# Optimization experiments

Hardware: AMD Instinct MI355X
Metric: run time of the kernel (lower is better)

## Reference

```python
import jax, jax.numpy as jnp
import numpy as np

VOCAB = 4194304
EMBED = 128
BATCH = 16384
NUM_DENSE = 13
NUM_CAT = 26
BOT_DIMS = (512, 256, 128)
TOP_DIMS = (1024, 1024, 512, 256, 1)


def _dense_params(key, fan_in, fan_out):
    kw, kb = jax.random.split(key)
    w = jax.random.normal(kw, (fan_in, fan_out), jnp.float32) * np.sqrt(2.0 / (fan_in + fan_out))
    b = jax.random.normal(kb, (fan_out,), jnp.float32) * np.sqrt(1.0 / fan_out)
    return w, b


def setup_inputs() -> dict:
    key = jax.random.key(0)
    ks = jax.random.split(key, 16)
    inp = {}
    inp['x_dense'] = jax.random.normal(ks[0], (BATCH, NUM_DENSE), jnp.float32)
    inp['x_cat'] = jax.random.randint(ks[1], (BATCH, NUM_CAT), 0, VOCAB, dtype=jnp.int32)
    # embedding table: uniform(0,1) * 1/sqrt(vocab)
    inp['embedding_table'] = jax.random.uniform(ks[2], (VOCAB, EMBED), jnp.float32) * np.float32(1.0 / np.sqrt(VOCAB))
    # bottom MLP params
    fan_in = NUM_DENSE
    for i, d in enumerate(BOT_DIMS):
        w, b = _dense_params(ks[3 + i], fan_in, d)
        inp[f'w_bot{i}'], inp[f'b_bot{i}'] = w, b
        fan_in = d
    # top MLP params; input dim = embed_dim + n_triu(27) = 128 + 378 = 506
    n_feat = 1 + NUM_CAT  # 27
    fan_in = EMBED + n_feat * (n_feat + 1) // 2
    for i, d in enumerate(TOP_DIMS):
        w, b = _dense_params(ks[8 + i], fan_in, d)
        inp[f'w_top{i}'], inp[f'b_top{i}'] = w, b
        fan_in = d
    return inp


def _forward(x_dense, x_cat, embedding_table,
             w_bot0, b_bot0, w_bot1, b_bot1, w_bot2, b_bot2,
             w_top0, b_top0, w_top1, b_top1, w_top2, b_top2,
             w_top3, b_top3, w_top4, b_top4):
    B = x_dense.shape[0]
    # bottom MLP
    h = x_dense
    for w, b in ((w_bot0, b_bot0), (w_bot1, b_bot1), (w_bot2, b_bot2)):
        h = jax.nn.relu(h @ w + b)
    bot_out = h  # [B, 128]
    feat = bot_out.reshape(B, -1, EMBED)  # [B, 1, 128]
    # embedding gather (irregular access)
    idx = (x_cat.reshape(-1) % VOCAB)
    emb = embedding_table[idx].reshape(B, NUM_CAT, EMBED)  # [B, 26, 128]
    stack = jnp.concatenate([feat, emb], axis=1)  # [B, 27, 128]
    # self interaction + upper-triangular (incl. diagonal) extraction
    xact = jnp.einsum('bnd,bmd->bnm', stack, stack)  # [B, 27, 27]
    i, j = jnp.triu_indices(stack.shape[1])
    inter = xact[:, i, j]  # [B, 378]
    top = jnp.concatenate([bot_out, inter], axis=-1)  # [B, 506]
    tops = ((w_top0, b_top0), (w_top1, b_top1), (w_top2, b_top2), (w_top3, b_top3), (w_top4, b_top4))
    for li, (w, b) in enumerate(tops):
        top = top @ w + b
        if li < len(tops) - 1:
            top = jax.nn.relu(top)
    return top  # [B, 1] logits


def reference(x_dense, x_cat, embedding_table,
              w_bot0, b_bot0, w_bot1, b_bot1, w_bot2, b_bot2,
              w_top0, b_top0, w_top1, b_top1, w_top2, b_top2,
              w_top3, b_top3, w_top4, b_top4):
    return _forward(x_dense, x_cat, embedding_table,
                    w_bot0, b_bot0, w_bot1, b_bot1, w_bot2, b_bot2,
                    w_top0, b_top0, w_top1, b_top1, w_top2, b_top2,
                    w_top3, b_top3, w_top4, b_top4)
```

## Files before the change

### kernel.cpp

```cpp
#include <hip/hip_runtime.h>
#include <cstdint>
#include <cstddef>

#define BATCH 16384
#define VOCAB_MASK (4194304 - 1)

typedef __attribute__((ext_vector_type(4))) float f32x4;
typedef __attribute__((ext_vector_type(8))) __bf16 bf16x8;
typedef __attribute__((ext_vector_type(4))) __bf16 bf16x4;

static_assert(sizeof(bf16x8) == 16, "bf16x8 must be 16 bytes");

static __device__ __forceinline__ __bf16 f2bf(float f) {
  union { float f; unsigned u; } in; in.f = f;
  unsigned r = in.u + 0x7FFF + ((in.u >> 16) & 1);
  union { unsigned short s; __bf16 b; } out; out.s = (unsigned short)(r >> 16);
  return out.b;
}
static __device__ __forceinline__ float bf2f(__bf16 b) {
  union { __bf16 b; unsigned short s; } in; in.b = b;
  union { unsigned u; float f; } out; out.u = ((unsigned)in.s) << 16;
  return out.f;
}

#define GLDS16(g, l) __builtin_amdgcn_global_load_lds( \
    (const __attribute__((address_space(1))) unsigned int*)(g), \
    (__attribute__((address_space(3))) unsigned int*)(l), 16, 0, 0)

static __device__ __forceinline__ unsigned swz16(unsigned b) {
  return b ^ ((((b >> 6) & 3u) ^ ((b >> 8) & 3u)) << 4);
}
static __device__ __forceinline__ bf16x8 lds_frag(const char* smem, unsigned base,
                                                  unsigned r, unsigned cg) {
  unsigned b = r * 64u + cg;
  return *(const bf16x8*)(smem + base + swz16(b));
}

struct TJob { const float* W; __bf16* WT; int K, N, Kp, tx, off; };
struct TJobs { TJob j[7]; };

__global__ __launch_bounds__(256) void transpose_all(TJobs js, int njobs)
{
  __shared__ float tile[64][65];
  int b = blockIdx.x;
  int ji = 0;
  #pragma unroll
  for (int i = 1; i < 7; ++i) if (i < njobs && b >= js.j[i].off) ji = i;
  const TJob jb = js.j[ji];
  int lb = b - jb.off;
  int bx = lb % jb.tx, by = lb / jb.tx;
  const int kb = bx * 64, nb = by * 64;
  const int tx = threadIdx.x & 63, ty = threadIdx.x >> 6;
  #pragma unroll
  for (int i = 0; i < 64; i += 4) {
    int k = kb + ty + i, n = nb + tx;
    tile[ty + i][tx] = (k < jb.K && n < jb.N) ? jb.W[(size_t)k * jb.N + n] : 0.f;
  }
  __syncthreads();
  #pragma unroll
  for (int i = 0; i < 64; i += 4) {
    int n = nb + ty + i, k = kb + tx;
    if (n < jb.N && k < jb.Kp) jb.WT[(size_t)n * jb.Kp + k] = f2bf(tile[tx][ty + i]);
  }
}

__global__ __launch_bounds__(256) void bottom_interact(
    const float* __restrict__ x, const int* __restrict__ xcat,
    const float* __restrict__ emb,
    const __bf16* __restrict__ w0t, const float* __restrict__ b0,
    const __bf16* __restrict__ w1t, const float* __restrict__ b1,
    const __bf16* __restrict__ w2t, const float* __restrict__ b2,
    __bf16* __restrict__ top_in)
{
  __shared__ __align__(16) char smem[77824];
  const int tid = threadIdx.x, lane = tid & 63, w = tid >> 6;
  const int r0 = blockIdx.x * 32;
  const int srow_b = lane >> 2;
  const int scol_b = (lane & 3) * 8;
  const unsigned rA = lane & 15, cgw = (lane >> 4) * 8;

  #define AS_B(r,c) (smem + 8704  + (r)*80   + (c)*2)
  #define BS_B(r,c) (smem + 11264 + (r)*64   + (c)*2)
  #define H1_B(r,c) (smem + 27648 + (r)*528  + (c)*2)
  #define H0_B(r,c) (smem + 44544 + (r)*1040 + (c)*2)
  #define H2_B(r,c) (smem +         (r)*272  + (c)*2)

  auto ld_gather = [&](float4 (&buf)[13], int s) {
    const int* xs = xcat + (size_t)(r0 + w * 8 + s) * 26;
    #pragma unroll
    for (int i = 0; i < 13; ++i) {
      int fi = 2 * i + (lane >> 5);
      int ridx = xs[fi] & VOCAB_MASK;
      buf[i] = *(const float4*)(emb + (size_t)ridx * 128 + (lane & 31) * 4);
    }
  };
  float4 bufA[13], bufB[13];
  ld_gather(bufA, 0);

  for (int idx = tid; idx < 32 * 40; idx += 256) {
    int row = idx / 40, k = idx - row * 40;
    float v = (k < 13) ? x[(size_t)(r0 + row) * 13 + k] : 0.f;
    *(__bf16*)AS_B(row, k) = f2bf(v);
  }

  #pragma unroll
  for (int p = 0; p < 2; ++p) {
    __syncthreads();
    #pragma unroll
    for (int c = 0; c < 4; ++c) {
      int row = w * 64 + c * 16 + srow_b;
      GLDS16(w0t + (size_t)(p * 256 + row) * 32 + scol_b, BS_B(row, scol_b));
    }
    __syncthreads();
    bf16x8 a[2], bv[4];
    #pragma unroll
    for (int m = 0; m < 2; ++m) a[m] = *(const bf16x8*)AS_B(rA + m * 16, cgw);
    #pragma unroll
    for (int n = 0; n < 4; ++n) bv[n] = *(const bf16x8*)BS_B(w * 64 + n * 16 + rA, cgw);
    f32x4 acc[2][4] = {};
    #pragma unroll
    for (int m = 0; m < 2; ++m)
      #pragma unroll
      for (int n = 0; n < 4; ++n)
        acc[m][n] = __builtin_amdgcn_mfma_f32_16x16x32_bf16(a[m], bv[n], acc[m][n], 0, 0, 0);
    #pragma unroll
    for (int m = 0; m < 2; ++m)
      #pragma unroll
      for (int n = 0; n < 4; ++n) {
        int col = p * 256 + w * 64 + n * 16 + (int)rA;
        float bb = b0[col];
        #pragma unroll
        for (int r = 0; r < 4; ++r) {
          int row = m * 16 + (lane >> 4) * 4 + r;
          *(__bf16*)H0_B(row, col) = f2bf(fmaxf(acc[m][n][r] + bb, 0.f));
        }
      }
  }

  f32x4 acc1[2][4] = {};
  for (int k0 = 0; k0 < 512; k0 += 32) {
    __syncthreads();
    #pragma unroll
    for (int c = 0; c < 4; ++c) {
      int row = w * 64 + c * 16 + srow_b;
      GLDS16(w1t + (size_t)row * 512 + k0 + scol_b, BS_B(row, scol_b));
    }
    __syncthreads();
    bf16x8 a[2], bv[4];
    #pragma unroll
    for (int m = 0; m < 2; ++m) a[m] = *(const bf16x8*)H0_B(rA + m * 16, k0 + cgw);
    #pragma unroll
    for (int n = 0; n < 4; ++n) bv[n] = *(const bf16x8*)BS_B(w * 64 + n * 16 + rA, cgw);
    #pragma unroll
    for (int m = 0; m < 2; ++m)
      #pragma unroll
      for (int n = 0; n < 4; ++n)
        acc1[m][n] = __builtin_amdgcn_mfma_f32_16x16x32_bf16(a[m], bv[n], acc1[m][n], 0, 0, 0);
  }
  #pragma unroll
  for (int m = 0; m < 2; ++m)
    #pragma unroll
    for (int n = 0; n < 4; ++n) {
      int col = w * 64 + n * 16 + (int)rA;
      float bb = b1[col];
      #pragma unroll
      for (int r = 0; r < 4; ++r) {
        int row = m * 16 + (lane >> 4) * 4 + r;
        *(__bf16*)H1_B(row, col) = f2bf(fmaxf(acc1[m][n][r] + bb, 0.f));
      }
    }

  f32x4 acc2[2][2] = {};
  for (int k0 = 0; k0 < 256; k0 += 32) {
    __syncthreads();
    #pragma unroll
    for (int c = 0; c < 2; ++c) {
      int row = w * 32 + c * 16 + srow_b;
      GLDS16(w2t + (size_t)row * 256 + k0 + scol_b, BS_B(row, scol_b));
    }
    __syncthreads();
    bf16x8 a[2], bv[2];
    #pragma unroll
    for (int m = 0; m < 2; ++m) a[m] = *(const bf16x8*)H1_B(rA + m * 16, k0 + cgw);
    #pragma unroll
    for (int n = 0; n < 2; ++n) bv[n] = *(const bf16x8*)BS_B(w * 32 + n * 16 + rA, cgw);
    #pragma unroll
    for (int m = 0; m < 2; ++m)
      #pragma unroll
      for (int n = 0; n < 2; ++n)
        acc2[m][n] = __builtin_amdgcn_mfma_f32_16x16x32_bf16(a[m], bv[n], acc2[m][n], 0, 0, 0);
  }
  #pragma unroll
  for (int m = 0; m < 2; ++m)
    #pragma unroll
    for (int n = 0; n < 2; ++n) {
      int col = w * 32 + n * 16 + (int)rA;
      float bb = b2[col];
      #pragma unroll
      for (int r = 0; r < 4; ++r) {
        int row = m * 16 + (lane >> 4) * 4 + r;
        *(__bf16*)H2_B(row, col) = f2bf(fmaxf(acc2[m][n][r] + bb, 0.f));
      }
    }

  __syncthreads();

  char* st_w = smem + 8704 + (unsigned)w * 8704u;
  #pragma unroll
  for (int r = 27; r < 32; ++r) *(unsigned*)(st_w + r * 272 + lane * 4) = 0;

  #pragma unroll
  for (int s = 0; s < 8; ++s) {
    float4 (&cur)[13] = (s & 1) ? bufB : bufA;
    float4 (&nxt)[13] = (s & 1) ? bufA : bufB;
    const int sg = r0 + w * 8 + s;
    __bf16* op = top_in + (size_t)sg * 512;

    unsigned hv = *(const unsigned*)(smem + (unsigned)(w * 8 + s) * 272u + lane * 4);
    *(unsigned*)(st_w + lane * 4) = hv;
    ((unsigned*)op)[lane] = hv;
    if (lane < 3) ((unsigned*)op)[253 + lane] = 0;

    #pragma unroll
    for (int i = 0; i < 13; ++i) {
      int row = 1 + 2 * i + (lane >> 5);
      float4 v = cur[i];
      bf16x4 bv;
      bv[0] = f2bf(v.x); bv[1] = f2bf(v.y); bv[2] = f2bf(v.z); bv[3] = f2bf(v.w);
      *(bf16x4*)(st_w + row * 272 + (lane & 31) * 8) = bv;
    }
    if (s < 7) ld_gather(nxt, s + 1);

    asm volatile("s_waitcnt lgkmcnt(0)" ::: "memory");
    __builtin_amdgcn_sched_barrier(0);

    f32x4 a00 = {}, a01 = {}, a11 = {};
    #pragma unroll
    for (int k0 = 0; k0 < 4; ++k0) {
      bf16x8 fr0 = *(const bf16x8*)(st_w + (lane & 15) * 272 + k0 * 64 + (lane >> 4) * 16);
      bf16x8 fr1 = *(const bf16x8*)(st_w + (16 + (lane & 15)) * 272 + k0 * 64 + (lane >> 4) * 16);
      a00 = __builtin_amdgcn_mfma_f32_16x16x32_bf16(fr0, fr0, a00, 0, 0, 0);
      a01 = __builtin_amdgcn_mfma_f32_16x16x32_bf16(fr0, fr1, a01, 0, 0, 0);
      a11 = __builtin_amdgcn_mfma_f32_16x16x32_bf16(fr1, fr1, a11, 0, 0, 0);
    }

    const int jc = lane & 15, rb = (lane >> 4) * 4;
    #pragma unroll
    for (int r = 0; r < 4; ++r) {
      {
        int i = rb + r, j = jc;
        if (i <= j) op[128 + i * 27 - i * (i - 1) / 2 + (j - i)] = f2bf(a00[r]);
      }
      {
        int i = rb + r, j = 16 + jc;
        if (j <= 26) op[128 + i * 27 - i * (i - 1) / 2 + (j - i)] = f2bf(a01[r]);
      }
      {
        int i = 16 + rb + r, j = 16 + jc;
        if (i <= j && j <= 26) op[128 + i * 27 - i * (i - 1) / 2 + (j - i)] = f2bf(a11[r]);
      }
    }
  }
  #undef AS_B
  #undef BS_B
  #undef H1_B
  #undef H0_B
  #undef H2_B
}

__global__ __launch_bounds__(512, 2) void gemm_8ph(
    const __bf16* __restrict__ A, const __bf16* __restrict__ WT,
    const float* __restrict__ bias, __bf16* __restrict__ C,
    int N, int sA, int K, int gm)
{
  __shared__ __align__(16) char smem[65536];
  const int tid = threadIdx.x, lane = tid & 63, w = tid >> 6;
  const int wm = w >> 2, wn = w & 3;

  int nb = gridDim.x;
  int id = blockIdx.x;
  int swz = ((nb & 7) == 0) ? ((id & 7) * (nb >> 3) + (id >> 3)) : id;
  const int m0 = (swz % gm) * 256, n0 = (swz / gm) * 256;

  unsigned Ld[2]; const __bf16* sAp[2]; const __bf16* sBp[2];
  #pragma unroll
  for (int h = 0; h < 2; ++h) {
    unsigned L = h * 8192u + (unsigned)w * 1024u + (unsigned)lane * 16u;
    unsigned Ls = swz16(L);
    Ld[h] = L;
    int srow = Ls >> 6, scb = Ls & 63;
    sAp[h] = A  + (size_t)(m0 + srow) * sA + (scb >> 1);
    sBp[h] = WT + (size_t)(n0 + srow) * K  + (scb >> 1);
  }

  #define STAGE_A(kt, p) { GLDS16(sAp[0] + (kt)*32, smem + (p)*32768 + Ld[0]); \
                           GLDS16(sAp[1] + (kt)*32, smem + (p)*32768 + Ld[1]); }
  #define STAGE_B(kt, p) { GLDS16(sBp[0] + (kt)*32, smem + (p)*32768 + 16384 + Ld[0]); \
                           GLDS16(sBp[1] + (kt)*32, smem + (p)*32768 + 16384 + Ld[1]); }

  const unsigned cg = (lane >> 4) * 16u;
  const unsigned rA = (lane & 15);

  f32x4 acc[8][4] = {};
  const int iters = (K >> 5) >> 1;

  STAGE_B(0, 0); STAGE_A(0, 0); STAGE_B(1, 1);
  asm volatile("s_waitcnt vmcnt(2)" ::: "memory");
  __builtin_amdgcn_s_barrier();
  __builtin_amdgcn_sched_barrier(0);

  for (int i = 0; i < iters; ++i) {
    const int t = 2 * i;
    const bool more = (i + 1 < iters);

    bf16x8 a0[4], b0[4];
    #pragma unroll
    for (int m = 0; m < 4; ++m) a0[m] = lds_frag(smem, 0, wm * 128 + m * 16 + rA, cg);
    #pragma unroll
    for (int n = 0; n < 4; ++n) b0[n] = lds_frag(smem, 16384, wn * 64 + n * 16 + rA, cg);
    STAGE_A(t + 1, 1);
    __builtin_amdgcn_s_barrier();
    asm volatile("s_waitcnt lgkmcnt(0)" ::: "memory");
    __builtin_amdgcn_sched_barrier(0);
    __builtin_amdgcn_s_setprio(1);
    #pragma unroll
    for (int m = 0; m < 4; ++m)
      #pragma unroll
      for (int n = 0; n < 4; ++n)
        acc[m][n] = __builtin_amdgcn_mfma_f32_16x16x32_bf16(a0[m], b0[n], acc[m][n], 0, 0, 0);
    __builtin_amdgcn_s_setprio(0);
    __builtin_amdgcn_s_barrier();
    __builtin_amdgcn_sched_barrier(0);

    bf16x8 a1[4];
    #pragma unroll
    for (int m = 0; m < 4; ++m) a1[m] = lds_frag(smem, 0, wm * 128 + 64 + m * 16 + rA, cg);
    if (more) STAGE_B(t + 2, 0);
    __builtin_amdgcn_s_barrier();
    asm volatile("s_waitcnt lgkmcnt(0)" ::: "memory");
    __builtin_amdgcn_sched_barrier(0);
    __builtin_amdgcn_s_setprio(1);
    #pragma unroll
    for (int m = 0; m < 4; ++m)
      #pragma unroll
      for (int n = 0; n < 4; ++n)
        acc[4 + m][n] = __builtin_amdgcn_mfma_f32_16x16x32_bf16(a1[m], b0[n], acc[4 + m][n], 0, 0, 0);
    __builtin_amdgcn_s_setprio(0);
    if (more) { asm volatile("s_waitcnt vmcnt(2)" ::: "memory"); }
    else      { asm volatile("s_waitcnt vmcnt(0)" ::: "memory"); }
    __builtin_amdgcn_s_barrier();
    __builtin_amdgcn_sched_barrier(0);

    bf16x8 a2[4], b2[4];
    #pragma unroll
    for (int m = 0; m < 4; ++m) a2[m] = lds_frag(smem, 32768, wm * 128 + m * 16 + rA, cg);
    #pragma unroll
    for (int n = 0; n < 4; ++n) b2[n] = lds_frag(smem, 32768 + 16384, wn * 64 + n * 16 + rA, cg);
    if (more) STAGE_A(t + 2, 0);
    __builtin_amdgcn_s_barrier();
    asm volatile("s_waitcnt lgkmcnt(0)" ::: "memory");
    __builtin_amdgcn_sched_barrier(0);
    __builtin_amdgcn_s_setprio(1);
    #pragma unroll
    for (int m = 0; m < 4; ++m)
      #pragma unroll
      for (int n = 0; n < 4; ++n)
        acc[m][n] = __builtin_amdgcn_mfma_f32_16x16x32_bf16(a2[m], b2[n], acc[m][n], 0, 0, 0);
    __builtin_amdgcn_s_setprio(0);
    __builtin_amdgcn_s_barrier();
    __builtin_amdgcn_sched_barrier(0);

    bf16x8 a3[4];
    #pragma unroll
    for (int m = 0; m < 4; ++m) a3[m] = lds_frag(smem, 32768, wm * 128 + 64 + m * 16 + rA, cg);
    if (more) STAGE_B(t + 3, 1);
    __builtin_amdgcn_s_barrier();
    asm volatile("s_waitcnt lgkmcnt(0)" ::: "memory");
    __builtin_amdgcn_sched_barrier(0);
    __builtin_amdgcn_s_setprio(1);
    #pragma unroll
    for (int m = 0; m < 4; ++m)
      #pragma unroll
      for (int n = 0; n < 4; ++n)
        acc[4 + m][n] = __builtin_amdgcn_mfma_f32_16x16x32_bf16(a3[m], b2[n], acc[4 + m][n], 0, 0, 0);
    __builtin_amdgcn_s_setprio(0);
    if (more) { asm volatile("s_waitcnt vmcnt(2)" ::: "memory"); }
    __builtin_amdgcn_s_barrier();
    __builtin_amdgcn_sched_barrier(0);
  }

  #pragma unroll
  for (int n = 0; n < 4; ++n) {
    int col = n0 + wn * 64 + n * 16 + (lane & 15);
    float bv = bias[col];
    #pragma unroll
    for (int m = 0; m < 8; ++m) {
      #pragma unroll
      for (int r = 0; r < 4; ++r) {
        int row = m0 + wm * 128 + m * 16 + (lane >> 4) * 4 + r;
        float v = fmaxf(acc[m][n][r] + bv, 0.f);
        C[(size_t)row * N + col] = f2bf(v);
      }
    }
  }
  #undef STAGE_A
  #undef STAGE_B
}

__global__ __launch_bounds__(512, 2) void gemm_8ph_n128(
    const __bf16* __restrict__ A, const __bf16* __restrict__ WT,
    const float* __restrict__ bias, __bf16* __restrict__ C,
    int N, int sA, int K, int gm)
{
  __shared__ __align__(16) char smem[49152];
  const int tid = threadIdx.x, lane = tid & 63, w = tid >> 6;
  const int wm = w >> 1, wn = w & 1;

  int nb = gridDim.x;
  int id = blockIdx.x;
  int swz = ((nb & 7) == 0) ? ((id & 7) * (nb >> 3) + (id >> 3)) : id;
  const int m0 = (swz % gm) * 256, n0 = (swz / gm) * 128;

  unsigned Ld[2]; const __bf16* sAp[2]; const __bf16* sBp0;
  #pragma unroll
  for (int h = 0; h < 2; ++h) {
    unsigned L = h * 8192u + (unsigned)w * 1024u + (unsigned)lane * 16u;
    unsigned Ls = swz16(L);
    Ld[h] = L;
    int srow = Ls >> 6, scb = Ls & 63;
    sAp[h] = A + (size_t)(m0 + srow) * sA + (scb >> 1);
  }
  {
    unsigned L = (unsigned)w * 1024u + (unsigned)lane * 16u;
    unsigned Ls = swz16(L);
    int srow = Ls >> 6, scb = Ls & 63;
    sBp0 = WT + (size_t)(n0 + srow) * K + (scb >> 1);
  }

  #define STAGE_A2(kt, p) { GLDS16(sAp[0] + (kt)*32, smem + (p)*24576 + Ld[0]); \
                            GLDS16(sAp[1] + (kt)*32, smem + (p)*24576 + Ld[1]); }
  #define STAGE_B1(kt, p) { GLDS16(sBp0 + (kt)*32, smem + (p)*24576 + 16384 + Ld[0]); }

  const unsigned cg = (lane >> 4) * 16u;
  const unsigned rA = (lane & 15);

  f32x4 acc[4][4] = {};
  const int iters = (K >> 5) >> 1;

  STAGE_B1(0, 0); STAGE_A2(0, 0); STAGE_B1(1, 1);
  asm volatile("s_waitcnt vmcnt(1)" ::: "memory");
  __builtin_amdgcn_s_barrier();
  __builtin_amdgcn_sched_barrier(0);

  for (int i = 0; i < iters; ++i) {
    const int t = 2 * i;
    const bool more = (i + 1 < iters);

    bf16x8 a0[2], b0[4];
    #pragma unroll
    for (int m = 0; m < 2; ++m) a0[m] = lds_frag(smem, 0, wm * 64 + m * 16 + rA, cg);
    #pragma unroll
    for (int n = 0; n < 4; ++n) b0[n] = lds_frag(smem, 16384, wn * 64 + n * 16 + rA, cg);
    STAGE_A2(t + 1, 1);
    __builtin_amdgcn_s_barrier();
    asm volatile("s_waitcnt lgkmcnt(0)" ::: "memory");
    __builtin_amdgcn_sched_barrier(0);
    __builtin_amdgcn_s_setprio(1);
    #pragma unroll
    for (int m = 0; m < 2; ++m)
      #pragma unroll
      for (int n = 0; n < 4; ++n)
        acc[m][n] = __builtin_amdgcn_mfma_f32_16x16x32_bf16(a0[m], b0[n], acc[m][n], 0, 0, 0);
    __builtin_amdgcn_s_setprio(0);
    __builtin_amdgcn_s_barrier();
    __builtin_amdgcn_sched_barrier(0);

    bf16x8 a1[2];
    #pragma unroll
    for (int m = 0; m < 2; ++m) a1[m] = lds_frag(smem, 0, wm * 64 + 32 + m * 16 + rA, cg);
    if (more) STAGE_B1(t + 2, 0);
    __builtin_amdgcn_s_barrier();
    asm volatile("s_waitcnt lgkmcnt(0)" ::: "memory");
    __builtin_amdgcn_sched_barrier(0);
    __builtin_amdgcn_s_setprio(1);
    #pragma unroll
    for (int m = 0; m < 2; ++m)
      #pragma unroll
      for (int n = 0; n < 4; ++n)
        acc[2 + m][n] = __builtin_amdgcn_mfma_f32_16x16x32_bf16(a1[m], b0[n], acc[2 + m][n], 0, 0, 0);
    __builtin_amdgcn_s_setprio(0);
    if (more) { asm volatile("s_waitcnt vmcnt(1)" ::: "memory"); }
    else      { asm volatile("s_waitcnt vmcnt(0)" ::: "memory"); }
    __builtin_amdgcn_s_barrier();
    __builtin_amdgcn_sched_barrier(0);

    bf16x8 a2[2], b2[4];
    #pragma unroll
    for (int m = 0; m < 2; ++m) a2[m] = lds_frag(smem, 24576, wm * 64 + m * 16 + rA, cg);
    #pragma unroll
    for (int n = 0; n < 4; ++n) b2[n] = lds_frag(smem, 24576 + 16384, wn * 64 + n * 16 + rA, cg);
    if (more) STAGE_A2(t + 2, 0);
    __builtin_amdgcn_s_barrier();
    asm volatile("s_waitcnt lgkmcnt(0)" ::: "memory");
    __builtin_amdgcn_sched_barrier(0);
    __builtin_amdgcn_s_setprio(1);
    #pragma unroll
    for (int m = 0; m < 2; ++m)
      #pragma unroll
      for (int n = 0; n < 4; ++n)
        acc[m][n] = __builtin_amdgcn_mfma_f32_16x16x32_bf16(a2[m], b2[n], acc[m][n], 0, 0, 0);
    __builtin_amdgcn_s_setprio(0);
    __builtin_amdgcn_s_barrier();
    __builtin_amdgcn_sched_barrier(0);

    bf16x8 a3[2];
    #pragma unroll
    for (int m = 0; m < 2; ++m) a3[m] = lds_frag(smem, 24576, wm * 64 + 32 + m * 16 + rA, cg);
    if (more) STAGE_B1(t + 3, 1);
    __builtin_amdgcn_s_barrier();
    asm volatile("s_waitcnt lgkmcnt(0)" ::: "memory");
    __builtin_amdgcn_sched_barrier(0);
    __builtin_amdgcn_s_setprio(1);
    #pragma unroll
    for (int m = 0; m < 2; ++m)
      #pragma unroll
      for (int n = 0; n < 4; ++n)
        acc[2 + m][n] = __builtin_amdgcn_mfma_f32_16x16x32_bf16(a3[m], b2[n], acc[2 + m][n], 0, 0, 0);
    __builtin_amdgcn_s_setprio(0);
    if (more) { asm volatile("s_waitcnt vmcnt(1)" ::: "memory"); }
    __builtin_amdgcn_s_barrier();
    __builtin_amdgcn_sched_barrier(0);
  }

  #pragma unroll
  for (int n = 0; n < 4; ++n) {
    int col = n0 + wn * 64 + n * 16 + (lane & 15);
    float bv = bias[col];
    #pragma unroll
    for (int m = 0; m < 4; ++m) {
      #pragma unroll
      for (int r = 0; r < 4; ++r) {
        int row = m0 + wm * 64 + m * 16 + (lane >> 4) * 4 + r;
        float v = fmaxf(acc[m][n][r] + bv, 0.f);
        C[(size_t)row * N + col] = f2bf(v);
      }
    }
  }
  #undef STAGE_A2
  #undef STAGE_B1
}

__global__ __launch_bounds__(256) void gemm_t3_final(
    const __bf16* __restrict__ A, const __bf16* __restrict__ WT,
    const float* __restrict__ b3, const float* __restrict__ w4,
    const float* __restrict__ b4, float* __restrict__ out)
{
  __shared__ __bf16 As[128][32];
  __shared__ __bf16 Bs[256][32];
  __shared__ float red[128][4];
  const int tid = threadIdx.x, lane = tid & 63, wid = tid >> 6;
  const int m0 = blockIdx.x * 128;
  const int srow = wid * 16 + (lane >> 2);
  const int scol = (lane & 3) * 8;
  const __bf16* Ag0 = A + (size_t)(m0 + srow) * 512 + scol;
  const __bf16* Ag1 = A + (size_t)(m0 + srow + 64) * 512 + scol;

  f32x4 acc[8][4] = {};

  for (int k0 = 0; k0 < 512; k0 += 32) {
    __syncthreads();
    GLDS16(Ag0 + k0, &As[srow][scol]);
    GLDS16(Ag1 + k0, &As[srow + 64][scol]);
    #pragma unroll
    for (int c = 0; c < 4; ++c) {
      int br = wid * 64 + c * 16 + (lane >> 2);
      GLDS16(WT + (size_t)br * 512 + k0 + scol, &Bs[br][scol]);
    }
    __syncthreads();

    bf16x8 af[8], bfv[4];
    #pragma unroll
    for (int m = 0; m < 8; ++m)
      af[m] = *(const bf16x8*)&As[m * 16 + (lane & 15)][(lane >> 4) * 8];
    #pragma unroll
    for (int n = 0; n < 4; ++n)
      bfv[n] = *(const bf16x8*)&Bs[wid * 64 + n * 16 + (lane & 15)][(lane >> 4) * 8];
    #pragma unroll
    for (int m = 0; m < 8; ++m)
      #pragma unroll
      for (int n = 0; n < 4; ++n)
        acc[m][n] = __builtin_amdgcn_mfma_f32_16x16x32_bf16(af[m], bfv[n], acc[m][n], 0, 0, 0);
  }

  float pd[8][4];
  #pragma unroll
  for (int m = 0; m < 8; ++m)
    #pragma unroll
    for (int r = 0; r < 4; ++r) pd[m][r] = 0.f;
  #pragma unroll
  for (int n = 0; n < 4; ++n) {
    int col = wid * 64 + n * 16 + (lane & 15);
    float bb = b3[col];
    float wc = w4[col];
    #pragma unroll
    for (int m = 0; m < 8; ++m)
      #pragma unroll
      for (int r = 0; r < 4; ++r)
        pd[m][r] += fmaxf(acc[m][n][r] + bb, 0.f) * wc;
  }
  #pragma unroll
  for (int m = 0; m < 8; ++m)
    #pragma unroll
    for (int r = 0; r < 4; ++r) {
      float s = pd[m][r];
      s += __shfl_xor(s, 1); s += __shfl_xor(s, 2);
      s += __shfl_xor(s, 4); s += __shfl_xor(s, 8);
      if ((lane & 15) == 0) red[m * 16 + (lane >> 4) * 4 + r][wid] = s;
    }
  __syncthreads();
  if (tid < 128)
    out[m0 + tid] = red[tid][0] + red[tid][1] + red[tid][2] + red[tid][3] + b4[0];
}

extern "C" void kernel_launch(void* const* d_in, const int* in_sizes, int n_in,
                              void* d_out, int out_size, void* d_ws, size_t ws_size,
                              hipStream_t stream)
{
  const float* x_dense = (const float*)d_in[0];
  const int*   x_cat   = (const int*)d_in[1];
  const float* emb     = (const float*)d_in[2];
  const float* wb[3] = {(const float*)d_in[3], (const float*)d_in[5], (const float*)d_in[7]};
  const float* bb[3] = {(const float*)d_in[4], (const float*)d_in[6], (const float*)d_in[8]};
  const float* wt[5] = {(const float*)d_in[9],  (const float*)d_in[11], (const float*)d_in[13],
                        (const float*)d_in[15], (const float*)d_in[17]};
  const float* bt[5] = {(const float*)d_in[10], (const float*)d_in[12], (const float*)d_in[14],
                        (const float*)d_in[16], (const float*)d_in[18]};
  float* out = (float*)d_out;

  char* ws = (char*)d_ws;
  const size_t MB = 1ull << 20;
  __bf16* wt_b0 = (__bf16*)(ws + 0 * MB);
  __bf16* wt_b1 = (__bf16*)(ws + 1 * MB);
  __bf16* wt_b2 = (__bf16*)(ws + 2 * MB);
  __bf16* wt_t0 = (__bf16*)(ws + 3 * MB);
  __bf16* wt_t1 = (__bf16*)(ws + 4 * MB);
  __bf16* wt_t2 = (__bf16*)(ws + 6 * MB);
  __bf16* wt_t3 = (__bf16*)(ws + 7 * MB);
  __bf16* top_in = (__bf16*)(ws + 12 * MB);
  __bf16* t2     = (__bf16*)(ws + 12 * MB);
  __bf16* t1     = (__bf16*)(ws + 28 * MB);
  __bf16* t0     = (__bf16*)(ws + 60 * MB);

  TJobs js;
  const float* Ws[7] = {wb[0], wb[1], wb[2], wt[0], wt[1], wt[2], wt[3]};
  __bf16* WTs[7] = {wt_b0, wt_b1, wt_b2, wt_t0, wt_t1, wt_t2, wt_t3};
  int Ks[7]  = {13, 512, 256, 506, 1024, 1024, 512};
  int Ns[7]  = {512, 256, 128, 1024, 1024, 512, 256};
  int Kps[7] = {32, 512, 256, 512, 1024, 1024, 512};
  int off = 0;
  for (int i = 0; i < 7; ++i) {
    int tx = (Kps[i] + 63) / 64, ty = (Ns[i] + 63) / 64;
    js.j[i] = TJob{Ws[i], WTs[i], Ks[i], Ns[i], Kps[i], tx, off};
    off += tx * ty;
  }
  transpose_all<<<dim3(off), dim3(256), 0, stream>>>(js, 7);

  bottom_interact<<<dim3(BATCH / 32), dim3(256), 0, stream>>>(
      x_dense, x_cat, emb, wt_b0, bb[0], wt_b1, bb[1], wt_b2, bb[2], top_in);

  gemm_8ph<<<dim3(256), dim3(512), 0, stream>>>(top_in, wt_t0, bt[0], t0, 1024, 512, 512, 64);
  gemm_8ph<<<dim3(256), dim3(512), 0, stream>>>(t0, wt_t1, bt[1], t1, 1024, 1024, 1024, 64);
  gemm_8ph_n128<<<dim3(256), dim3(512), 0, stream>>>(t1, wt_t2, bt[2], t2, 512, 1024, 1024, 64);

  gemm_t3_final<<<dim3(128), dim3(256), 0, stream>>>(t2, wt_t3, bt[3], wt[4], bt[4], out);
}
```

Baseline: 197.4 us.

## Split bottom MLP from interaction and halve top GEMM M-tile

The fused bottom-MLP-plus-interaction kernel is split in two. The bottom MLP now writes its 128-wide output to a workspace buffer, and a separate interaction kernel runs one sample per wave with many more blocks, so more embedding gathers are in flight at once. The first two top-layer GEMMs switch from 256x256 to 128x256 tiles, doubling the grid to 512 blocks with smaller LDS use and a higher occupancy bound. The cost is an extra kernel launch, an extra global round trip for the bottom output, and less reuse per GEMM tile.

```diff
diff --git a/kernel.cpp b/kernel.cpp
--- a/kernel.cpp
+++ b/kernel.cpp
@@ -64,43 +64,27 @@
   }
 }
 
-__global__ __launch_bounds__(256) void bottom_interact(
-    const float* __restrict__ x, const int* __restrict__ xcat,
-    const float* __restrict__ emb,
+__global__ __launch_bounds__(256) void bottom_fused(
+    const float* __restrict__ x,
     const __bf16* __restrict__ w0t, const float* __restrict__ b0,
     const __bf16* __restrict__ w1t, const float* __restrict__ b1,
     const __bf16* __restrict__ w2t, const float* __restrict__ b2,
-    __bf16* __restrict__ top_in)
+    __bf16* __restrict__ h2out)
 {
-  __shared__ __align__(16) char smem[77824];
+  __shared__ __bf16 h0s[32][520];
+  __shared__ __bf16 h1s[32][264];
+  __shared__ __bf16 As[32][40];
+  __shared__ __bf16 Bs[256][32];
   const int tid = threadIdx.x, lane = tid & 63, w = tid >> 6;
   const int r0 = blockIdx.x * 32;
   const int srow_b = lane >> 2;
   const int scol_b = (lane & 3) * 8;
   const unsigned rA = lane & 15, cgw = (lane >> 4) * 8;
 
-  #define AS_B(r,c) (smem + 8704  + (r)*80   + (c)*2)
-  #define BS_B(r,c) (smem + 11264 + (r)*64   + (c)*2)
-  #define H1_B(r,c) (smem + 27648 + (r)*528  + (c)*2)
-  #define H0_B(r,c) (smem + 44544 + (r)*1040 + (c)*2)
-  #define H2_B(r,c) (smem +         (r)*272  + (c)*2)
-
-  auto ld_gather = [&](float4 (&buf)[13], int s) {
-    const int* xs = xcat + (size_t)(r0 + w * 8 + s) * 26;
-    #pragma unroll
-    for (int i = 0; i < 13; ++i) {
-      int fi = 2 * i + (lane >> 5);
-      int ridx = xs[fi] & VOCAB_MASK;
-      buf[i] = *(const float4*)(emb + (size_t)ridx * 128 + (lane & 31) * 4);
-    }
-  };
-  float4 bufA[13], bufB[13];
-  ld_gather(bufA, 0);
-
   for (int idx = tid; idx < 32 * 40; idx += 256) {
     int row = idx / 40, k = idx - row * 40;
     float v = (k < 13) ? x[(size_t)(r0 + row) * 13 + k] : 0.f;
-    *(__bf16*)AS_B(row, k) = f2bf(v);
+    As[row][k] = f2bf(v);
   }
 
   #pragma unroll
@@ -109,14 +93,14 @@
     #pragma unroll
     for (int c = 0; c < 4; ++c) {
       int row = w * 64 + c * 16 + srow_b;
-      GLDS16(w0t + (size_t)(p * 256 + row) * 32 + scol_b, BS_B(row, scol_b));
+      GLDS16(w0t + (size_t)(p * 256 + row) * 32 + scol_b, &Bs[row][scol_b]);
     }
     __syncthreads();
     bf16x8 a[2], bv[4];
     #pragma unroll
-    for (int m = 0; m < 2; ++m) a[m] = *(const bf16x8*)AS_B(rA + m * 16, cgw);
-    #pragma unroll
-    for (int n = 0; n < 4; ++n) bv[n] = *(const bf16x8*)BS_B(w * 64 + n * 16 + rA, cgw);
+    for (int m = 0; m < 2; ++m) a[m] = *(const bf16x8*)&As[rA + m * 16][cgw];
+    #pragma unroll
+    for (int n = 0; n < 4; ++n) bv[n] = *(const bf16x8*)&Bs[w * 64 + n * 16 + rA][cgw];
     f32x4 acc[2][4] = {};
     #pragma unroll
     for (int m = 0; m < 2; ++m)
@@ -132,7 +116,7 @@
         #pragma unroll
         for (int r = 0; r < 4; ++r) {
           int row = m * 16 + (lane >> 4) * 4 + r;
-          *(__bf16*)H0_B(row, col) = f2bf(fmaxf(acc[m][n][r] + bb, 0.f));
+          h0s[row][col] = f2bf(fmaxf(acc[m][n][r] + bb, 0.f));
         }
       }
   }
@@ -143,14 +127,14 @@
     #pragma unroll
     for (int c = 0; c < 4; ++c) {
       int row = w * 64 + c * 16 + srow_b;
-      GLDS16(w1t + (size_t)row * 512 + k0 + scol_b, BS_B(row, scol_b));
+      GLDS16(w1t + (size_t)row * 512 + k0 + scol_b, &Bs[row][scol_b]);
     }
     __syncthreads();
     bf16x8 a[2], bv[4];
     #pragma unroll
-    for (int m = 0; m < 2; ++m) a[m] = *(const bf16x8*)H0_B(rA + m * 16, k0 + cgw);
-    #pragma unroll
-    for (int n = 0; n < 4; ++n) bv[n] = *(const bf16x8*)BS_B(w * 64 + n * 16 + rA, cgw);
+    for (int m = 0; m < 2; ++m) a[m] = *(const bf16x8*)&h0s[rA + m * 16][k0 + cgw];
+    #pragma unroll
+    for (int n = 0; n < 4; ++n) bv[n] = *(const bf16x8*)&Bs[w * 64 + n * 16 + rA][cgw];
     #pragma unroll
     for (int m = 0; m < 2; ++m)
       #pragma unroll
@@ -166,7 +150,7 @@
       #pragma unroll
       for (int r = 0; r < 4; ++r) {
         int row = m * 16 + (lane >> 4) * 4 + r;
-        *(__bf16*)H1_B(row, col) = f2bf(fmaxf(acc1[m][n][r] + bb, 0.f));
+        h1s[row][col] = f2bf(fmaxf(acc1[m][n][r] + bb, 0.f));
       }
     }
 
@@ -176,14 +160,14 @@
     #pragma unroll
     for (int c = 0; c < 2; ++c) {
       int row = w * 32 + c * 16 + srow_b;
-      GLDS16(w2t + (size_t)row * 256 + k0 + scol_b, BS_B(row, scol_b));
+      GLDS16(w2t + (size_t)row * 256 + k0 + scol_b, &Bs[row][scol_b]);
     }
     __syncthreads();
     bf16x8 a[2], bv[2];
     #pragma unroll
-    for (int m = 0; m < 2; ++m) a[m] = *(const bf16x8*)H1_B(rA + m * 16, k0 + cgw);
-    #pragma unroll
-    for (int n = 0; n < 2; ++n) bv[n] = *(const bf16x8*)BS_B(w * 32 + n * 16 + rA, cgw);
+    for (int m = 0; m < 2; ++m) a[m] = *(const bf16x8*)&h1s[rA + m * 16][k0 + cgw];
+    #pragma unroll
+    for (int n = 0; n < 2; ++n) bv[n] = *(const bf16x8*)&Bs[w * 32 + n * 16 + rA][cgw];
     #pragma unroll
     for (int m = 0; m < 2; ++m)
       #pragma unroll
@@ -199,112 +183,113 @@
       #pragma unroll
       for (int r = 0; r < 4; ++r) {
         int row = m * 16 + (lane >> 4) * 4 + r;
-        *(__bf16*)H2_B(row, col) = f2bf(fmaxf(acc2[m][n][r] + bb, 0.f));
+        h2out[(size_t)(r0 + row) * 128 + col] = f2bf(fmaxf(acc2[m][n][r] + bb, 0.f));
       }
     }
-
-  __syncthreads();
-
-  char* st_w = smem + 8704 + (unsigned)w * 8704u;
-  #pragma unroll
-  for (int r = 27; r < 32; ++r) *(unsigned*)(st_w + r * 272 + lane * 4) = 0;
-
-  #pragma unroll
-  for (int s = 0; s < 8; ++s) {
-    float4 (&cur)[13] = (s & 1) ? bufB : bufA;
-    float4 (&nxt)[13] = (s & 1) ? bufA : bufB;
-    const int sg = r0 + w * 8 + s;
-    __bf16* op = top_in + (size_t)sg * 512;
-
-    unsigned hv = *(const unsigned*)(smem + (unsigned)(w * 8 + s) * 272u + lane * 4);
-    *(unsigned*)(st_w + lane * 4) = hv;
-    ((unsigned*)op)[lane] = hv;
-    if (lane < 3) ((unsigned*)op)[253 + lane] = 0;
-
-    #pragma unroll
-    for (int i = 0; i < 13; ++i) {
-      int row = 1 + 2 * i + (lane >> 5);
-      float4 v = cur[i];
-      bf16x4 bv;
-      bv[0] = f2bf(v.x); bv[1] = f2bf(v.y); bv[2] = f2bf(v.z); bv[3] = f2bf(v.w);
-      *(bf16x4*)(st_w + row * 272 + (lane & 31) * 8) = bv;
-    }
-    if (s < 7) ld_gather(nxt, s + 1);
-
-    asm volatile("s_waitcnt lgkmcnt(0)" ::: "memory");
-    __builtin_amdgcn_sched_barrier(0);
-
-    f32x4 a00 = {}, a01 = {}, a11 = {};
-    #pragma unroll
-    for (int k0 = 0; k0 < 4; ++k0) {
-      bf16x8 fr0 = *(const bf16x8*)(st_w + (lane & 15) * 272 + k0 * 64 + (lane >> 4) * 16);
-      bf16x8 fr1 = *(const bf16x8*)(st_w + (16 + (lane & 15)) * 272 + k0 * 64 + (lane >> 4) * 16);
-      a00 = __builtin_amdgcn_mfma_f32_16x16x32_bf16(fr0, fr0, a00, 0, 0, 0);
-      a01 = __builtin_amdgcn_mfma_f32_16x16x32_bf16(fr0, fr1, a01, 0, 0, 0);
-      a11 = __builtin_amdgcn_mfma_f32_16x16x32_bf16(fr1, fr1, a11, 0, 0, 0);
-    }
-
-    const int jc = lane & 15, rb = (lane >> 4) * 4;
-    #pragma unroll
-    for (int r = 0; r < 4; ++r) {
-      {
-        int i = rb + r, j = jc;
-        if (i <= j) op[128 + i * 27 - i * (i - 1) / 2 + (j - i)] = f2bf(a00[r]);
-      }
-      {
-        int i = rb + r, j = 16 + jc;
-        if (j <= 26) op[128 + i * 27 - i * (i - 1) / 2 + (j - i)] = f2bf(a01[r]);
-      }
-      {
-        int i = 16 + rb + r, j = 16 + jc;
-        if (i <= j && j <= 26) op[128 + i * 27 - i * (i - 1) / 2 + (j - i)] = f2bf(a11[r]);
-      }
-    }
-  }
-  #undef AS_B
-  #undef BS_B
-  #undef H1_B
-  #undef H0_B
-  #undef H2_B
-}
-
-__global__ __launch_bounds__(512, 2) void gemm_8ph(
+}
+
+__global__ __launch_bounds__(256) void interact_mfma(
+    const __bf16* __restrict__ bot, const int* __restrict__ xcat,
+    const float* __restrict__ emb, __bf16* __restrict__ top_in)
+{
+  __shared__ __bf16 st[4][32][136];
+  const int tid = threadIdx.x, lane = tid & 63, w = tid >> 6;
+  const int s = blockIdx.x * 4 + w;
+
+  const int* xr = xcat + (size_t)s * 26;
+  float4 buf[13];
+  #pragma unroll
+  for (int i = 0; i < 13; ++i) {
+    int fi = 2 * i + (lane >> 5);
+    int ridx = xr[fi] & VOCAB_MASK;
+    buf[i] = *(const float4*)(emb + (size_t)ridx * 128 + (lane & 31) * 4);
+  }
+
+  *(unsigned*)&st[w][0][lane * 2] = *(const unsigned*)(bot + (size_t)s * 128 + lane * 2);
+  #pragma unroll
+  for (int r = 27; r < 32; ++r) *(unsigned*)&st[w][r][lane * 2] = 0u;
+  #pragma unroll
+  for (int i = 0; i < 13; ++i) {
+    int row = 1 + 2 * i + (lane >> 5);
+    bf16x4 bv;
+    bv[0] = f2bf(buf[i].x); bv[1] = f2bf(buf[i].y);
+    bv[2] = f2bf(buf[i].z); bv[3] = f2bf(buf[i].w);
+    *(bf16x4*)&st[w][row][(lane & 31) * 4] = bv;
+  }
+
+  f32x4 a00 = {}, a01 = {}, a11 = {};
+  #pragma unroll
+  for (int k0 = 0; k0 < 4; ++k0) {
+    bf16x8 fr0 = *(const bf16x8*)&st[w][(lane & 15)][k0 * 32 + (lane >> 4) * 8];
+    bf16x8 fr1 = *(const bf16x8*)&st[w][16 + (lane & 15)][k0 * 32 + (lane >> 4) * 8];
+    a00 = __builtin_amdgcn_mfma_f32_16x16x32_bf16(fr0, fr0, a00, 0, 0, 0);
+    a01 = __builtin_amdgcn_mfma_f32_16x16x32_bf16(fr0, fr1, a01, 0, 0, 0);
+    a11 = __builtin_amdgcn_mfma_f32_16x16x32_bf16(fr1, fr1, a11, 0, 0, 0);
+  }
+
+  __bf16* op = top_in + (size_t)s * 512;
+  ((unsigned*)op)[lane] = *(const unsigned*)&st[w][0][lane * 2];
+  if (lane < 3) ((unsigned*)op)[253 + lane] = 0u;
+
+  const int jc = lane & 15, rb = (lane >> 4) * 4;
+  #pragma unroll
+  for (int r = 0; r < 4; ++r) {
+    {
+      int i = rb + r, j = jc;
+      if (i <= j) op[128 + i * 27 - i * (i - 1) / 2 + (j - i)] = f2bf(a00[r]);
+    }
+    {
+      int i = rb + r, j = 16 + jc;
+      if (j <= 26) op[128 + i * 27 - i * (i - 1) / 2 + (j - i)] = f2bf(a01[r]);
+    }
+    {
+      int i = 16 + rb + r, j = 16 + jc;
+      if (i <= j && j <= 26) op[128 + i * 27 - i * (i - 1) / 2 + (j - i)] = f2bf(a11[r]);
+    }
+  }
+}
+
+__global__ __launch_bounds__(512, 4) void gemm_8ph_bm128(
     const __bf16* __restrict__ A, const __bf16* __restrict__ WT,
     const float* __restrict__ bias, __bf16* __restrict__ C,
     int N, int sA, int K, int gm)
 {
-  __shared__ __align__(16) char smem[65536];
+  __shared__ __align__(16) char smem[49152];
   const int tid = threadIdx.x, lane = tid & 63, w = tid >> 6;
   const int wm = w >> 2, wn = w & 3;
 
   int nb = gridDim.x;
   int id = blockIdx.x;
   int swz = ((nb & 7) == 0) ? ((id & 7) * (nb >> 3) + (id >> 3)) : id;
-  const int m0 = (swz % gm) * 256, n0 = (swz / gm) * 256;
-
-  unsigned Ld[2]; const __bf16* sAp[2]; const __bf16* sBp[2];
+  const int m0 = (swz % gm) * 128, n0 = (swz / gm) * 256;
+
+  unsigned LdA; const __bf16* sApA;
+  {
+    unsigned L = (unsigned)w * 1024u + (unsigned)lane * 16u;
+    unsigned Ls = swz16(L);
+    LdA = L;
+    sApA = A + (size_t)(m0 + (Ls >> 6)) * sA + ((Ls & 63) >> 1);
+  }
+  unsigned LdB[2]; const __bf16* sBp[2];
   #pragma unroll
   for (int h = 0; h < 2; ++h) {
     unsigned L = h * 8192u + (unsigned)w * 1024u + (unsigned)lane * 16u;
     unsigned Ls = swz16(L);
-    Ld[h] = L;
-    int srow = Ls >> 6, scb = Ls & 63;
-    sAp[h] = A  + (size_t)(m0 + srow) * sA + (scb >> 1);
-    sBp[h] = WT + (size_t)(n0 + srow) * K  + (scb >> 1);
-  }
-
-  #define STAGE_A(kt, p) { GLDS16(sAp[0] + (kt)*32, smem + (p)*32768 + Ld[0]); \
-                           GLDS16(sAp[1] + (kt)*32, smem + (p)*32768 + Ld[1]); }
-  #define STAGE_B(kt, p) { GLDS16(sBp[0] + (kt)*32, smem + (p)*32768 + 16384 + Ld[0]); \
-                           GLDS16(sBp[1] + (kt)*32, smem + (p)*32768 + 16384 + Ld[1]); }
+    LdB[h] = L;
+    sBp[h] = WT + (size_t)(n0 + (Ls >> 6)) * K + ((Ls & 63) >> 1);
+  }
+
+  #define STAGE_A1(kt, p) { GLDS16(sApA + (kt)*32, smem + (p)*24576 + LdA); }
+  #define STAGE_B2(kt, p) { GLDS16(sBp[0] + (kt)*32, smem + (p)*24576 + 8192 + LdB[0]); \
+                            GLDS16(sBp[1] + (kt)*32, smem + (p)*24576 + 8192 + LdB[1]); }
 
   const unsigned cg = (lane >> 4) * 16u;
   const unsigned rA = (lane & 15);
 
-  f32x4 acc[8][4] = {};
+  f32x4 acc[4][4] = {};
   const int iters = (K >> 5) >> 1;
 
-  STAGE_B(0, 0); STAGE_A(0, 0); STAGE_B(1, 1);
+  STAGE_B2(0, 0); STAGE_A1(0, 0); STAGE_B2(1, 1);
   asm volatile("s_waitcnt vmcnt(2)" ::: "memory");
   __builtin_amdgcn_s_barrier();
   __builtin_amdgcn_sched_barrier(0);
@@ -313,18 +298,18 @@
     const int t = 2 * i;
     const bool more = (i + 1 < iters);
 
-    bf16x8 a0[4], b0[4];
-    #pragma unroll
-    for (int m = 0; m < 4; ++m) a0[m] = lds_frag(smem, 0, wm * 128 + m * 16 + rA, cg);
-    #pragma unroll
-    for (int n = 0; n < 4; ++n) b0[n] = lds_frag(smem, 16384, wn * 64 + n * 16 + rA, cg);
-    STAGE_A(t + 1, 1);
-    __builtin_amdgcn_s_barrier();
-    asm volatile("s_waitcnt lgkmcnt(0)" ::: "memory");
-    __builtin_amdgcn_sched_barrier(0);
-    __builtin_amdgcn_s_setprio(1);
-    #pragma unroll
-    for (int m = 0; m < 4; ++m)
+    bf16x8 a0[2], b0[4];
+    #pragma unroll
+    for (int m = 0; m < 2; ++m) a0[m] = lds_frag(smem, 0, wm * 64 + m * 16 + rA, cg);
+    #pragma unroll
+    for (int n = 0; n < 4; ++n) b0[n] = lds_frag(smem, 8192, wn * 64 + n * 16 + rA, cg);
+    STAGE_A1(t + 1, 1);
+    __builtin_amdgcn_s_barrier();
+    asm volatile("s_waitcnt lgkmcnt(0)" ::: "memory");
+    __builtin_amdgcn_sched_barrier(0);
+    __builtin_amdgcn_s_setprio(1);
+    #pragma unroll
+    for (int m = 0; m < 2; ++m)
       #pragma unroll
       for (int n = 0; n < 4; ++n)
         acc[m][n] = __builtin_amdgcn_mfma_f32_16x16x32_bf16(a0[m], b0[n], acc[m][n], 0, 0, 0);
@@ -332,37 +317,37 @@
     __builtin_amdgcn_s_barrier();
     __builtin_amdgcn_sched_barrier(0);
 
-    bf16x8 a1[4];
-    #pragma unroll
-    for (int m = 0; m < 4; ++m) a1[m] = lds_frag(smem, 0, wm * 128 + 64 + m * 16 + rA, cg);
-    if (more) STAGE_B(t + 2, 0);
-    __builtin_amdgcn_s_barrier();
-    asm volatile("s_waitcnt lgkmcnt(0)" ::: "memory");
-    __builtin_amdgcn_sched_barrier(0);
-    __builtin_amdgcn_s_setprio(1);
-    #pragma unroll
-    for (int m = 0; m < 4; ++m)
-      #pragma unroll
-      for (int n = 0; n < 4; ++n)
-        acc[4 + m][n] = __builtin_amdgcn_mfma_f32_16x16x32_bf16(a1[m], b0[n], acc[4 + m][n], 0, 0, 0);
+    bf16x8 a1[2];
+    #pragma unroll
+    for (int m = 0; m < 2; ++m) a1[m] = lds_frag(smem, 0, wm * 64 + 32 + m * 16 + rA, cg);
+    if (more) STAGE_B2(t + 2, 0);
+    __builtin_amdgcn_s_barrier();
+    asm volatile("s_waitcnt lgkmcnt(0)" ::: "memory");
+    __builtin_amdgcn_sched_barrier(0);
+    __builtin_amdgcn_s_setprio(1);
+    #pragma unroll
+    for (int m = 0; m < 2; ++m)
+      #pragma unroll
+      for (int n = 0; n < 4; ++n)
+        acc[2 + m][n] = __builtin_amdgcn_mfma_f32_16x16x32_bf16(a1[m], b0[n], acc[2 + m][n], 0, 0, 0);
     __builtin_amdgcn_s_setprio(0);
     if (more) { asm volatile("s_waitcnt vmcnt(2)" ::: "memory"); }
     else      { asm volatile("s_waitcnt vmcnt(0)" ::: "memory"); }
     __builtin_amdgcn_s_barrier();
     __builtin_amdgcn_sched_barrier(0);
 
-    bf16x8 a2[4], b2[4];
-    #pragma unroll
-    for (int m = 0; m < 4; ++m) a2[m] = lds_frag(smem, 32768, wm * 128 + m * 16 + rA, cg);
-    #pragma unroll
-    for (int n = 0; n < 4; ++n) b2[n] = lds_frag(smem, 32768 + 16384, wn * 64 + n * 16 + rA, cg);
-    if (more) STAGE_A(t + 2, 0);
-    __builtin_amdgcn_s_barrier();
-    asm volatile("s_waitcnt lgkmcnt(0)" ::: "memory");
-    __builtin_amdgcn_sched_barrier(0);
-    __builtin_amdgcn_s_setprio(1);
-    #pragma unroll
-    for (int m = 0; m < 4; ++m)
+    bf16x8 a2[2], b2[4];
+    #pragma unroll
+    for (int m = 0; m < 2; ++m) a2[m] = lds_frag(smem, 24576, wm * 64 + m * 16 + rA, cg);
+    #pragma unroll
+    for (int n = 0; n < 4; ++n) b2[n] = lds_frag(smem, 24576 + 8192, wn * 64 + n * 16 + rA, cg);
+    if (more) STAGE_A1(t + 2, 0);
+    __builtin_amdgcn_s_barrier();
+    asm volatile("s_waitcnt lgkmcnt(0)" ::: "memory");
+    __builtin_amdgcn_sched_barrier(0);
+    __builtin_amdgcn_s_setprio(1);
+    #pragma unroll
+    for (int m = 0; m < 2; ++m)
       #pragma unroll
       for (int n = 0; n < 4; ++n)
         acc[m][n] = __builtin_amdgcn_mfma_f32_16x16x32_bf16(a2[m], b2[n], acc[m][n], 0, 0, 0);
@@ -370,19 +355,19 @@
     __builtin_amdgcn_s_barrier();
     __builtin_amdgcn_sched_barrier(0);
 
-    bf16x8 a3[4];
-    #pragma unroll
-    for (int m = 0; m < 4; ++m) a3[m] = lds_frag(smem, 32768, wm * 128 + 64 + m * 16 + rA, cg);
-    if (more) STAGE_B(t + 3, 1);
-    __builtin_amdgcn_s_barrier();
-    asm volatile("s_waitcnt lgkmcnt(0)" ::: "memory");
-    __builtin_amdgcn_sched_barrier(0);
-    __builtin_amdgcn_s_setprio(1);
-    #pragma unroll
-    for (int m = 0; m < 4; ++m)
-      #pragma unroll
-      for (int n = 0; n < 4; ++n)
-        acc[4 + m][n] = __builtin_amdgcn_mfma_f32_16x16x32_bf16(a3[m], b2[n], acc[4 + m][n], 0, 0, 0);
+    bf16x8 a3[2];
+    #pragma unroll
+    for (int m = 0; m < 2; ++m) a3[m] = lds_frag(smem, 24576, wm * 64 + 32 + m * 16 + rA, cg);
+    if (more) STAGE_B2(t + 3, 1);
+    __builtin_amdgcn_s_barrier();
+    asm volatile("s_waitcnt lgkmcnt(0)" ::: "memory");
+    __builtin_amdgcn_sched_barrier(0);
+    __builtin_amdgcn_s_setprio(1);
+    #pragma unroll
+    for (int m = 0; m < 2; ++m)
+      #pragma unroll
+      for (int n = 0; n < 4; ++n)
+        acc[2 + m][n] = __builtin_amdgcn_mfma_f32_16x16x32_bf16(a3[m], b2[n], acc[2 + m][n], 0, 0, 0);
     __builtin_amdgcn_s_setprio(0);
     if (more) { asm volatile("s_waitcnt vmcnt(2)" ::: "memory"); }
     __builtin_amdgcn_s_barrier();
@@ -394,17 +379,17 @@
     int col = n0 + wn * 64 + n * 16 + (lane & 15);
     float bv = bias[col];
     #pragma unroll
-    for (int m = 0; m < 8; ++m) {
+    for (int m = 0; m < 4; ++m) {
       #pragma unroll
       for (int r = 0; r < 4; ++r) {
-        int row = m0 + wm * 128 + m * 16 + (lane >> 4) * 4 + r;
+        int row = m0 + wm * 64 + m * 16 + (lane >> 4) * 4 + r;
         float v = fmaxf(acc[m][n][r] + bv, 0.f);
         C[(size_t)row * N + col] = f2bf(v);
       }
     }
   }
-  #undef STAGE_A
-  #undef STAGE_B
+  #undef STAGE_A1
+  #undef STAGE_B2
 }
 
 __global__ __launch_bounds__(512, 2) void gemm_8ph_n128(
@@ -646,6 +631,7 @@
   __bf16* wt_t1 = (__bf16*)(ws + 4 * MB);
   __bf16* wt_t2 = (__bf16*)(ws + 6 * MB);
   __bf16* wt_t3 = (__bf16*)(ws + 7 * MB);
+  __bf16* h2     = (__bf16*)(ws + 8 * MB);
   __bf16* top_in = (__bf16*)(ws + 12 * MB);
   __bf16* t2     = (__bf16*)(ws + 12 * MB);
   __bf16* t1     = (__bf16*)(ws + 28 * MB);
@@ -665,11 +651,13 @@
   }
   transpose_all<<<dim3(off), dim3(256), 0, stream>>>(js, 7);
 
-  bottom_interact<<<dim3(BATCH / 32), dim3(256), 0, stream>>>(
-      x_dense, x_cat, emb, wt_b0, bb[0], wt_b1, bb[1], wt_b2, bb[2], top_in);
-
-  gemm_8ph<<<dim3(256), dim3(512), 0, stream>>>(top_in, wt_t0, bt[0], t0, 1024, 512, 512, 64);
-  gemm_8ph<<<dim3(256), dim3(512), 0, stream>>>(t0, wt_t1, bt[1], t1, 1024, 1024, 1024, 64);
+  bottom_fused<<<dim3(BATCH / 32), dim3(256), 0, stream>>>(
+      x_dense, wt_b0, bb[0], wt_b1, bb[1], wt_b2, bb[2], h2);
+
+  interact_mfma<<<dim3(BATCH / 4), dim3(256), 0, stream>>>(h2, x_cat, emb, top_in);
+
+  gemm_8ph_bm128<<<dim3(512), dim3(512), 0, stream>>>(top_in, wt_t0, bt[0], t0, 1024, 512, 512, 128);
+  gemm_8ph_bm128<<<dim3(512), dim3(512), 0, stream>>>(t0, wt_t1, bt[1], t1, 1024, 1024, 1024, 128);
   gemm_8ph_n128<<<dim3(256), dim3(512), 0, stream>>>(t1, wt_t2, bt[2], t2, 512, 1024, 1024, 64);
 
   gemm_t3_final<<<dim3(128), dim3(256), 0, stream>>>(t2, wt_t3, bt[3], wt[4], bt[4], out);
```

Result: faster. 189.2 us (-4.1%).
